# Kernel tuning notes

Measured on AMD Instinct MI355X. Metric: run time of the kernel, lower is better.

The kernel has to match this reference:

```python
import jax, jax.numpy as jnp
import numpy as np

N = 4096   # num ROIs across the batch (sgdet: ~8 images x 512 proposals)
H = 256    # rl_input_size == rl_hidden_size (hard-coded in __init__)
C = 151    # Visual Genome object classes incl. background


def setup_inputs() -> dict:
    key = jax.random.key(0)
    ks = jax.random.split(key, 7)
    prepro_feat = jax.random.normal(ks[0], (N, H), jnp.float32)
    d = jax.random.uniform(ks[1], (N, C), jnp.float32)
    obj_distributions = d / d.sum(-1, keepdims=True)  # softmax-like class probs
    co_occour = jax.random.uniform(ks[2], (C, C), jnp.float32)
    W_sub = jax.random.normal(ks[3], (H, H), jnp.float32) / np.sqrt(H)
    b_sub = jnp.zeros((H,), jnp.float32)
    W_obj = jax.random.normal(ks[4], (H, H), jnp.float32) / np.sqrt(H)
    b_obj = jnp.zeros((H,), jnp.float32)
    w_scores = jax.random.normal(ks[5], (3 * H + 3,), jnp.float32) / np.sqrt(3 * H + 3)
    b_scores = jnp.zeros((), jnp.float32)
    return dict(prepro_feat=prepro_feat, obj_distributions=obj_distributions,
                co_occour=co_occour, W_sub=W_sub, b_sub=b_sub,
                W_obj=W_obj, b_obj=b_obj, w_scores=w_scores, b_scores=b_scores)


def reference(prepro_feat, obj_distributions, co_occour, W_sub, b_sub,
              W_obj, b_obj, w_scores, b_scores):
    n = prepro_feat.shape[0]
    h = W_sub.shape[1]
    # label_scores = co_occour.sum(1)
    label_scores = co_occour.sum(1)                                   # [C]
    # rl_sub/rl_obj Linear + ReLU. In the torch expand, pair (i,j) uses sub[j], obj[i].
    sub = jax.nn.relu(prepro_feat @ W_sub + b_sub)                    # [N,H]
    obj = jax.nn.relu(prepro_feat @ W_obj + b_obj)                    # [N,H]
    # pair_score[i,j] = sum_{a,b} dist[j,a] * dist[i,b] * co[a,b]  (detached)
    pair_score = jax.lax.stop_gradient(
        jnp.einsum('ja,ab,ib->ij', obj_distributions, co_occour, obj_distributions))  # [N,N]
    s = jax.lax.stop_gradient(obj_distributions @ label_scores)       # [N]
    sub_score = s[None, :]   # varies along j
    obj_score = s[:, None]   # varies along i
    # rl_scores Linear over concat(sub*obj, sub, obj, pair, sub_score, obj_score),
    # decomposed exactly into its blocks (avoids the [N,N,3H+3] intermediate).
    w_mul, w_s, w_o = w_scores[:h], w_scores[h:2 * h], w_scores[2 * h:3 * h]
    w_ps, w_ss, w_os = w_scores[3 * h], w_scores[3 * h + 1], w_scores[3 * h + 2]
    pair_out = ((obj * w_mul) @ sub.T                                 # [i,j] = sum_h obj[i,h]*sub[j,h]*w_mul[h]
                + (sub @ w_s)[None, :]
                + (obj @ w_o)[:, None]
                + w_ps * pair_score + w_ss * sub_score + w_os * obj_score
                + b_scores)                                           # [N,N]
    pair_gates = jax.nn.sigmoid(pair_out).reshape(-1, 1)              # [N*N, 1]
    return pair_gates
```

## Files before the change

### kernel.cpp

```cpp
#include <hip/hip_runtime.h>
#include <hip/hip_bf16.h>
#include <math.h>

#define N_DIM 4096
#define H_DIM 256
#define C_DIM 151
#define KP    448
#define KT    160

typedef unsigned short ushort_t;
typedef __attribute__((ext_vector_type(8))) short bf16x8;
typedef __attribute__((ext_vector_type(4))) float f32x4;

#define WSB_PPACK  0
#define WSB_WT     2097152
#define WSB_DPACK  2359296
#define WSB_COT    3670016
#define WSB_PART   3731456
#define WSB_SPART  3993600
#define WSB_APACK  4091904
#define WSB_BPACK  7761920

#define GLL(src, dst) __builtin_amdgcn_global_load_lds( \
    (const __attribute__((address_space(1))) void*)(src), \
    (__attribute__((address_space(3))) void*)(dst), 16, 0, 0)

__global__ __launch_bounds__(256) void k_cvt(
    const float* __restrict__ P, const float* __restrict__ Ws,
    const float* __restrict__ Wo, const float* __restrict__ D,
    const float* __restrict__ co, const float* __restrict__ wsc,
    __hip_bfloat16* __restrict__ Pp, __hip_bfloat16* __restrict__ Wt,
    __hip_bfloat16* __restrict__ Dpack, __hip_bfloat16* __restrict__ coT,
    __hip_bfloat16* __restrict__ Apack) {
    __shared__ float shbuf[64 * C_DIM];
    const int t = threadIdx.x;
    const int bid = blockIdx.x;
    if (bid < 512) {
        int idx = (bid * 256 + t) * 8;
        float4 a = *(const float4*)(P + idx);
        float4 b = *(const float4*)(P + idx + 4);
        __hip_bfloat16 h[8];
        h[0] = __float2bfloat16(a.x); h[1] = __float2bfloat16(a.y);
        h[2] = __float2bfloat16(a.z); h[3] = __float2bfloat16(a.w);
        h[4] = __float2bfloat16(b.x); h[5] = __float2bfloat16(b.y);
        h[6] = __float2bfloat16(b.z); h[7] = __float2bfloat16(b.w);
        *(bf16x8*)&Pp[idx] = *(bf16x8*)h;
    } else if (bid < 544) {
        const int b  = bid - 512;
        const int k0 = (b & 3) * 64;
        const int h0 = ((b >> 2) & 3) * 64;
        const int z  = b >> 4;
        const float* W = z ? Wo : Ws;
        #pragma unroll
        for (int q = 0; q < 4; ++q) {
            int r = (t >> 4) + q * 16;
            int c = (t & 15) * 4;
            float4 f = *(const float4*)&W[(size_t)(k0 + r) * H_DIM + h0 + c];
            shbuf[r * 65 + c] = f.x; shbuf[r * 65 + c + 1] = f.y;
            shbuf[r * 65 + c + 2] = f.z; shbuf[r * 65 + c + 3] = f.w;
        }
        __syncthreads();
        #pragma unroll
        for (int q = 0; q < 2; ++q) {
            int idx = t + q * 256;
            int h   = idx >> 3;
            int kc  = idx & 7;
            __hip_bfloat16 u[8];
            #pragma unroll
            for (int j = 0; j < 8; ++j)
                u[j] = __float2bfloat16(shbuf[(kc * 8 + j) * 65 + h]);
            *(bf16x8*)&Wt[((size_t)z * H_DIM + h0 + h) * H_DIM + k0 + kc * 8] = *(bf16x8*)u;
        }
    } else if (bid < 608) {
        const int b  = bid - 544;
        const int i0 = b * 64;
        for (int idx = t; idx < 64 * C_DIM; idx += 256)
            shbuf[idx] = D[(size_t)i0 * C_DIM + idx];
        __syncthreads();
        const float wps = wsc[768];
        for (int o = t; o < 64 * (KT / 8); o += 256) {
            int r = o / (KT / 8), ch = o % (KT / 8);
            __hip_bfloat16 u[8];
            #pragma unroll
            for (int j = 0; j < 8; ++j) {
                int k = ch * 8 + j;
                u[j] = __float2bfloat16(k < C_DIM ? shbuf[r * C_DIM + k] : 0.f);
            }
            *(bf16x8*)&Dpack[(size_t)(i0 + r) * KT + ch * 8] = *(bf16x8*)u;
        }
        for (int o = t; o < 64 * 24; o += 256) {
            int r = o / 24, ch = o % 24;
            __hip_bfloat16 u[8];
            #pragma unroll
            for (int j = 0; j < 8; ++j) {
                int c = ch * 8 + j;
                u[j] = __float2bfloat16(c < C_DIM ? wps * shbuf[r * C_DIM + c] : 0.f);
            }
            *(bf16x8*)&Apack[(size_t)(i0 + r) * KP + H_DIM + ch * 8] = *(bf16x8*)u;
        }
    } else {
        const int q  = bid - 608;
        const int a0 = (q % 3) * 64;
        const int c0 = (q / 3) * 64;
        for (int o = t; o < 64 * 64; o += 256) {
            int r = o >> 6, c = o & 63;
            float v = 0.f;
            if (a0 + r < C_DIM && c0 + c < C_DIM)
                v = co[(size_t)(a0 + r) * C_DIM + c0 + c];
            shbuf[r * 65 + c] = v;
        }
        __syncthreads();
        const int nch = (a0 == 128) ? 4 : 8;
        for (int o = t; o < 64 * 8; o += 256) {
            int cl = o >> 3, ch = o & 7;
            if (ch < nch) {
                __hip_bfloat16 u[8];
                #pragma unroll
                for (int j = 0; j < 8; ++j)
                    u[j] = __float2bfloat16(shbuf[(ch * 8 + j) * 65 + cl]);
                *(bf16x8*)&coT[(size_t)(c0 + cl) * KT + a0 + ch * 8] = *(bf16x8*)u;
            }
        }
    }
}

__global__ __launch_bounds__(256) void k_mid(
    const ushort_t* __restrict__ Pp, const ushort_t* __restrict__ Wt,
    const ushort_t* __restrict__ Dpack, const ushort_t* __restrict__ coT,
    const float* __restrict__ bsub, const float* __restrict__ bobj,
    const float* __restrict__ wsc,
    __hip_bfloat16* __restrict__ Apack, __hip_bfloat16* __restrict__ Bpack,
    float* __restrict__ part, float* __restrict__ spart) {
    __shared__ ushort_t As[128 * 256];
    __shared__ ushort_t Bs[64 * 256];

    const int t = threadIdx.x;
    const int w = t >> 6, l = t & 63;
    const int wr = w >> 1, wc = w & 1;
    const int lr = l & 15, g = l >> 4;
    const int bid = blockIdx.x;

    if (bid < 256) {
        const int hblk = bid & 3;
        const int i0   = ((bid >> 2) & 31) * 128;
        const int z    = bid >> 7;
        const int j0   = hblk * 64;
        const float* bias = z ? bobj : bsub;
        const ushort_t* Wz = Wt + (size_t)z * H_DIM * H_DIM;

        #pragma unroll
        for (int r_ = 0; r_ < 16; ++r_) {
            int idx = t + r_ * 256, row = idx >> 5, cl = idx & 31;
            int cs = cl ^ (row & 7);
            GLL(Pp + (size_t)(i0 + row) * H_DIM + cs * 8, &As[idx * 8]);
        }
        #pragma unroll
        for (int r_ = 0; r_ < 8; ++r_) {
            int idx = t + r_ * 256, row = idx >> 5, cl = idx & 31;
            int cs = cl ^ (row & 7);
            GLL(Wz + (size_t)(j0 + row) * H_DIM + cs * 8, &Bs[idx * 8]);
        }
        __syncthreads();

        f32x4 acc[4][2];
        #pragma unroll
        for (int m = 0; m < 4; ++m)
            #pragma unroll
            for (int n = 0; n < 2; ++n) acc[m][n] = f32x4{0.f, 0.f, 0.f, 0.f};

        #pragma unroll
        for (int ks2 = 0; ks2 < 8; ++ks2) {
            bf16x8 a[4], b[2];
            int c = ks2 * 4 + g;
            #pragma unroll
            for (int m = 0; m < 4; ++m) {
                int Rl = wr * 64 + m * 16 + lr;
                int cl = c ^ (Rl & 7);
                a[m] = *(const bf16x8*)&As[(Rl * 32 + cl) * 8];
            }
            #pragma unroll
            for (int n = 0; n < 2; ++n) {
                int Rl = wc * 32 + n * 16 + lr;
                int cl = c ^ (Rl & 7);
                b[n] = *(const bf16x8*)&Bs[(Rl * 32 + cl) * 8];
            }
            #pragma unroll
            for (int m = 0; m < 4; ++m)
                #pragma unroll
                for (int n = 0; n < 2; ++n)
                    acc[m][n] = __builtin_amdgcn_mfma_f32_16x16x32_bf16(
                        a[m], b[n], acc[m][n], 0, 0, 0);
        }

        int hn[2]; float bb[2], wse[2], wmu[2];
        #pragma unroll
        for (int n = 0; n < 2; ++n) {
            hn[n]  = j0 + wc * 32 + n * 16 + lr;
            bb[n]  = bias[hn[n]];
            wse[n] = wsc[(z ? 512 : 256) + hn[n]];
            wmu[n] = wsc[hn[n]];
        }
        float* partq = part + (size_t)(z * 8 + hblk * 2 + wc) * N_DIM;
        #pragma unroll
        for (int m = 0; m < 4; ++m) {
            float p[4] = {0.f, 0.f, 0.f, 0.f};
            #pragma unroll
            for (int n = 0; n < 2; ++n)
                #pragma unroll
                for (int r = 0; r < 4; ++r) {
                    float v = acc[m][n][r] + bb[n];
                    v = v > 0.f ? v : 0.f;
                    int i = i0 + wr * 64 + m * 16 + g * 4 + r;
                    if (z) Apack[(size_t)i * KP + hn[n]] = __float2bfloat16(v * wmu[n]);
                    else   Bpack[(size_t)i * KP + hn[n]] = __float2bfloat16(v);
                    p[r] += v * wse[n];
                }
            #pragma unroll
            for (int r = 0; r < 4; ++r) {
                p[r] += __shfl_xor(p[r], 1);
                p[r] += __shfl_xor(p[r], 2);
                p[r] += __shfl_xor(p[r], 4);
                p[r] += __shfl_xor(p[r], 8);
            }
            if (lr == 0)
                #pragma unroll
                for (int r = 0; r < 4; ++r)
                    partq[i0 + wr * 64 + m * 16 + g * 4 + r] = p[r];
        }
    } else {
        const int q  = bid - 256;
        const int j0 = (q % 3) * 64;
        const int i0 = (q / 3) * 64;

        bf16x8 a[2][5], b[2][5];
        #pragma unroll
        for (int m = 0; m < 2; ++m) {
            const ushort_t* ap = Dpack + (size_t)(i0 + wr * 32 + m * 16 + lr) * KT + g * 8;
            #pragma unroll
            for (int ks = 0; ks < 5; ++ks) a[m][ks] = *(const bf16x8*)(ap + ks * 32);
        }
        #pragma unroll
        for (int n = 0; n < 2; ++n) {
            const ushort_t* bp = coT + (size_t)(j0 + wc * 32 + n * 16 + lr) * KT + g * 8;
            #pragma unroll
            for (int ks = 0; ks < 5; ++ks) b[n][ks] = *(const bf16x8*)(bp + ks * 32);
        }

        f32x4 acc[2][2];
        #pragma unroll
        for (int m = 0; m < 2; ++m)
            #pragma unroll
            for (int n = 0; n < 2; ++n) acc[m][n] = f32x4{0.f, 0.f, 0.f, 0.f};
        #pragma unroll
        for (int ks = 0; ks < 5; ++ks)
            #pragma unroll
            for (int m = 0; m < 2; ++m)
                #pragma unroll
                for (int n = 0; n < 2; ++n)
                    acc[m][n] = __builtin_amdgcn_mfma_f32_16x16x32_bf16(
                        a[m][ks], b[n][ks], acc[m][n], 0, 0, 0);

        float* sp = spart + (size_t)((q % 3) * 2 + wc) * N_DIM;
        #pragma unroll
        for (int m = 0; m < 2; ++m) {
            float p[4] = {0.f, 0.f, 0.f, 0.f};
            #pragma unroll
            for (int n = 0; n < 2; ++n) {
                int col = j0 + wc * 32 + n * 16 + lr;
                #pragma unroll
                for (int r = 0; r < 4; ++r) {
                    int i = i0 + wr * 32 + m * 16 + g * 4 + r;
                    float v = acc[m][n][r];
                    Bpack[(size_t)i * KP + H_DIM + col] = __float2bfloat16(v);
                    p[r] += v;
                }
            }
            #pragma unroll
            for (int r = 0; r < 4; ++r) {
                p[r] += __shfl_xor(p[r], 1);
                p[r] += __shfl_xor(p[r], 2);
                p[r] += __shfl_xor(p[r], 4);
                p[r] += __shfl_xor(p[r], 8);
            }
            if (lr == 0)
                #pragma unroll
                for (int r = 0; r < 4; ++r)
                    sp[i0 + wr * 32 + m * 16 + g * 4 + r] = p[r];
        }
    }
}

__global__ __launch_bounds__(512, 2) void k_main(
    const ushort_t* __restrict__ Apack, const ushort_t* __restrict__ Bpack,
    const float* __restrict__ part, const float* __restrict__ spart,
    const float* __restrict__ wsc, const float* __restrict__ bsc,
    float* __restrict__ out) {
    __shared__ ushort_t pool[2][2][256 * 64];
    __shared__ float rbS[256], cbS[256];

    const int t = threadIdx.x;
    const int w = t >> 6, l = t & 63;
    const int wm = w >> 2, wn = w & 3;
    const int lr = l & 15, g = l >> 4;
    const int bid = blockIdx.x;
    const int swz = (bid & 7) * 32 + (bid >> 3);
    const int i0 = (swz >> 4) * 256;
    const int j0 = (swz & 15) * 256;

#define K_STAGE(buf, ks) do {                                                   \
    _Pragma("unroll")                                                           \
    for (int r_ = 0; r_ < 4; ++r_) {                                            \
        int idx_ = t + r_ * 512, row_ = idx_ >> 3, cl_ = idx_ & 7;              \
        int cs_ = cl_ ^ (row_ & 7);                                             \
        GLL(Apack + (size_t)(i0+row_)*KP + (ks)*64 + cs_*8, &pool[buf][0][idx_*8]); \
        GLL(Bpack + (size_t)(j0+row_)*KP + (ks)*64 + cs_*8, &pool[buf][1][idx_*8]); \
    }                                                                           \
} while (0)

#define K_COMPUTE(cur) do {                                                     \
    _Pragma("unroll")                                                           \
    for (int ks2 = 0; ks2 < 2; ++ks2) {                                         \
        bf16x8 a[8], b[4];                                                      \
        int c = ks2 * 4 + g;                                                    \
        _Pragma("unroll")                                                       \
        for (int m = 0; m < 8; ++m) {                                           \
            int Rl = wm * 128 + m * 16 + lr;                                    \
            int cl = c ^ (Rl & 7);                                              \
            a[m] = *(const bf16x8*)&pool[cur][0][(Rl * 8 + cl) * 8];            \
        }                                                                       \
        _Pragma("unroll")                                                       \
        for (int n = 0; n < 4; ++n) {                                           \
            int Rl = wn * 64 + n * 16 + lr;                                     \
            int cl = c ^ (Rl & 7);                                              \
            b[n] = *(const bf16x8*)&pool[cur][1][(Rl * 8 + cl) * 8];            \
        }                                                                       \
        _Pragma("unroll")                                                       \
        for (int m = 0; m < 8; ++m)                                             \
            _Pragma("unroll")                                                   \
            for (int n = 0; n < 4; ++n)                                         \
                acc[m][n] = __builtin_amdgcn_mfma_f32_16x16x32_bf16(            \
                    a[m], b[n], acc[m][n], 0, 0, 0);                            \
    }                                                                           \
} while (0)

    K_STAGE(0, 0);
    if (t < 256) {
        int i = i0 + t; float r = 0.f, si = 0.f;
        #pragma unroll
        for (int q = 8; q < 16; ++q) r += part[(size_t)q * N_DIM + i];
        #pragma unroll
        for (int q = 0; q < 6; ++q) si += spart[(size_t)q * N_DIM + i];
        rbS[t] = r + wsc[770] * si;
    } else {
        int j = j0 + (t - 256); float c = 0.f, sj = 0.f;
        #pragma unroll
        for (int q = 0; q < 8; ++q) c += part[(size_t)q * N_DIM + j];
        #pragma unroll
        for (int q = 0; q < 6; ++q) sj += spart[(size_t)q * N_DIM + j];
        cbS[t - 256] = c + wsc[769] * sj + bsc[0];
    }
    __syncthreads();

    f32x4 acc[8][4];
    #pragma unroll
    for (int m = 0; m < 8; ++m)
        #pragma unroll
        for (int n = 0; n < 4; ++n) acc[m][n] = f32x4{0.f, 0.f, 0.f, 0.f};

    for (int ks = 0; ks < 6; ++ks) {
        const int cur = ks & 1;
        K_STAGE(cur ^ 1, ks + 1);
        asm volatile("s_waitcnt vmcnt(8)" ::: "memory");
        __builtin_amdgcn_s_barrier();
        __builtin_amdgcn_sched_barrier(0);
        K_COMPUTE(cur);
        __builtin_amdgcn_s_barrier();
        __builtin_amdgcn_sched_barrier(0);
    }
    asm volatile("s_waitcnt vmcnt(0)" ::: "memory");
    __builtin_amdgcn_s_barrier();
    __builtin_amdgcn_sched_barrier(0);
    K_COMPUTE(0);
    __builtin_amdgcn_s_barrier();
    __builtin_amdgcn_sched_barrier(0);
#undef K_STAGE
#undef K_COMPUTE

    float cbv[4];
    #pragma unroll
    for (int n = 0; n < 4; ++n) cbv[n] = cbS[wn * 64 + n * 16 + lr];
    float* OutS = (float*)pool;
    #pragma unroll
    for (int m = 0; m < 8; ++m) {
        #pragma unroll
        for (int n = 0; n < 4; ++n) {
            #pragma unroll
            for (int r = 0; r < 4; ++r) {
                float rb = rbS[wm * 128 + m * 16 + g * 4 + r];
                float v  = acc[m][n][r] + rb + cbv[n];
                float e  = __expf(-v);
                OutS[(wm * 16 + g * 4 + r) * 260 + wn * 64 + n * 16 + lr] =
                    __builtin_amdgcn_rcpf(1.0f + e);
            }
        }
        asm volatile("s_waitcnt lgkmcnt(0)" ::: "memory");
        __builtin_amdgcn_s_barrier();
        __builtin_amdgcn_sched_barrier(0);
        {
            int rl = t >> 4, c16 = t & 15;
            int gr = i0 + (rl >> 4) * 128 + m * 16 + (rl & 15);
            float* op = out + (size_t)gr * N_DIM + j0;
            const float* rp = OutS + rl * 260;
            #pragma unroll
            for (int k = 0; k < 4; ++k) {
                float4 v4 = *(const float4*)(rp + (c16 + 16 * k) * 4);
                *(float4*)(op + (c16 + 16 * k) * 4) = v4;
            }
        }
        __builtin_amdgcn_s_barrier();
        __builtin_amdgcn_sched_barrier(0);
    }
}

extern "C" void kernel_launch(void* const* d_in, const int* in_sizes, int n_in,
                              void* d_out, int out_size, void* d_ws, size_t ws_size,
                              hipStream_t stream) {
    const float* prepro = (const float*)d_in[0];
    const float* D      = (const float*)d_in[1];
    const float* co     = (const float*)d_in[2];
    const float* Wsub   = (const float*)d_in[3];
    const float* bsub   = (const float*)d_in[4];
    const float* Wobj   = (const float*)d_in[5];
    const float* bobj   = (const float*)d_in[6];
    const float* wsc    = (const float*)d_in[7];
    const float* bsc    = (const float*)d_in[8];
    float* out = (float*)d_out;

    char* ws = (char*)d_ws;
    __hip_bfloat16* Ppack = (__hip_bfloat16*)(ws + WSB_PPACK);
    __hip_bfloat16* Wt    = (__hip_bfloat16*)(ws + WSB_WT);
    __hip_bfloat16* Dpack = (__hip_bfloat16*)(ws + WSB_DPACK);
    __hip_bfloat16* coT   = (__hip_bfloat16*)(ws + WSB_COT);
    float* part  = (float*)(ws + WSB_PART);
    float* spart = (float*)(ws + WSB_SPART);
    __hip_bfloat16* Apack = (__hip_bfloat16*)(ws + WSB_APACK);
    __hip_bfloat16* Bpack = (__hip_bfloat16*)(ws + WSB_BPACK);

    k_cvt<<<617, 256, 0, stream>>>(prepro, Wsub, Wobj, D, co, wsc,
                                   Ppack, Wt, Dpack, coT, Apack);
    k_mid<<<448, 256, 0, stream>>>(
        (const ushort_t*)Ppack, (const ushort_t*)Wt,
        (const ushort_t*)Dpack, (const ushort_t*)coT,
        bsub, bobj, wsc, Apack, Bpack, part, spart);
    k_main<<<256, 512, 0, stream>>>(
        (const ushort_t*)Apack, (const ushort_t*)Bpack, part, spart, wsc, bsc, out);
}
```

Before: 49.22 us.

## Interleave chunked global-to-LDS prefetch with MFMA phases in GEMM main loop

Splits each K-stage's async global-to-LDS copy into four chunks (two for B, two for A) and issues them between four MFMA sub-phases, instead of issuing the whole next stage at the top of the iteration. B fragments are kept in registers across the two M-halves, and s_setprio is raised around the MFMA bursts. The aim is to spread memory issue across compute and keep the matrix cores fed. The cost is many more workgroup barriers per iteration, which adds synchronisation overhead. The separate __syncthreads after the bias setup is also dropped.

```diff
diff --git a/kernel.cpp b/kernel.cpp
--- a/kernel.cpp
+++ b/kernel.cpp
@@ -307,43 +307,6 @@
     const int i0 = (swz >> 4) * 256;
     const int j0 = (swz & 15) * 256;
 
-#define K_STAGE(buf, ks) do {                                                   \
-    _Pragma("unroll")                                                           \
-    for (int r_ = 0; r_ < 4; ++r_) {                                            \
-        int idx_ = t + r_ * 512, row_ = idx_ >> 3, cl_ = idx_ & 7;              \
-        int cs_ = cl_ ^ (row_ & 7);                                             \
-        GLL(Apack + (size_t)(i0+row_)*KP + (ks)*64 + cs_*8, &pool[buf][0][idx_*8]); \
-        GLL(Bpack + (size_t)(j0+row_)*KP + (ks)*64 + cs_*8, &pool[buf][1][idx_*8]); \
-    }                                                                           \
-} while (0)
-
-#define K_COMPUTE(cur) do {                                                     \
-    _Pragma("unroll")                                                           \
-    for (int ks2 = 0; ks2 < 2; ++ks2) {                                         \
-        bf16x8 a[8], b[4];                                                      \
-        int c = ks2 * 4 + g;                                                    \
-        _Pragma("unroll")                                                       \
-        for (int m = 0; m < 8; ++m) {                                           \
-            int Rl = wm * 128 + m * 16 + lr;                                    \
-            int cl = c ^ (Rl & 7);                                              \
-            a[m] = *(const bf16x8*)&pool[cur][0][(Rl * 8 + cl) * 8];            \
-        }                                                                       \
-        _Pragma("unroll")                                                       \
-        for (int n = 0; n < 4; ++n) {                                           \
-            int Rl = wn * 64 + n * 16 + lr;                                     \
-            int cl = c ^ (Rl & 7);                                              \
-            b[n] = *(const bf16x8*)&pool[cur][1][(Rl * 8 + cl) * 8];            \
-        }                                                                       \
-        _Pragma("unroll")                                                       \
-        for (int m = 0; m < 8; ++m)                                             \
-            _Pragma("unroll")                                                   \
-            for (int n = 0; n < 4; ++n)                                         \
-                acc[m][n] = __builtin_amdgcn_mfma_f32_16x16x32_bf16(            \
-                    a[m], b[n], acc[m][n], 0, 0, 0);                            \
-    }                                                                           \
-} while (0)
-
-    K_STAGE(0, 0);
     if (t < 256) {
         int i = i0 + t; float r = 0.f, si = 0.f;
         #pragma unroll
@@ -359,7 +322,54 @@
         for (int q = 0; q < 6; ++q) sj += spart[(size_t)q * N_DIM + j];
         cbS[t - 256] = c + wsc[769] * sj + bsc[0];
     }
-    __syncthreads();
+
+#define STAGE_CHUNK(buf, ks, half, ab, basePtr, base0) do {                     \
+    _Pragma("unroll")                                                           \
+    for (int r_ = 0; r_ < 2; ++r_) {                                           \
+        int idx_ = t + (r_ + (half) * 2) * 512;                                 \
+        int row_ = idx_ >> 3, cl_ = idx_ & 7;                                   \
+        int cs_ = cl_ ^ (row_ & 7);                                             \
+        GLL(basePtr + (size_t)((base0) + row_) * KP + (ks) * 64 + cs_ * 8,      \
+            &pool[buf][ab][idx_ * 8]);                                          \
+    }                                                                           \
+} while (0)
+
+#define DS_B(ks2) do {                                                          \
+    _Pragma("unroll")                                                           \
+    for (int n_ = 0; n_ < 4; ++n_) {                                            \
+        int Rl = wn * 64 + n_ * 16 + lr;                                        \
+        int cl = ((ks2) * 4 + g) ^ (Rl & 7);                                    \
+        breg[ks2][n_] = *(const bf16x8*)&pool[cur][1][(Rl * 8 + cl) * 8];       \
+    }                                                                           \
+} while (0)
+
+#define DS_A(mh, ks2) do {                                                      \
+    _Pragma("unroll")                                                           \
+    for (int m_ = 0; m_ < 4; ++m_) {                                            \
+        int Rl = wm * 128 + (mh) * 64 + m_ * 16 + lr;                           \
+        int cl = ((ks2) * 4 + g) ^ (Rl & 7);                                    \
+        areg[m_] = *(const bf16x8*)&pool[cur][0][(Rl * 8 + cl) * 8];            \
+    }                                                                           \
+} while (0)
+
+#define MFMA16(mh, ks2) do {                                                    \
+    __builtin_amdgcn_s_setprio(1);                                              \
+    _Pragma("unroll")                                                           \
+    for (int m_ = 0; m_ < 4; ++m_)                                              \
+        _Pragma("unroll")                                                       \
+        for (int n_ = 0; n_ < 4; ++n_)                                          \
+            acc[(mh) * 4 + m_][n_] = __builtin_amdgcn_mfma_f32_16x16x32_bf16(   \
+                areg[m_], breg[ks2][n_], acc[(mh) * 4 + m_][n_], 0, 0, 0);      \
+    __builtin_amdgcn_s_setprio(0);                                              \
+} while (0)
+
+#define BAR() do { __builtin_amdgcn_s_barrier();                                \
+                   __builtin_amdgcn_sched_barrier(0); } while (0)
+
+    STAGE_CHUNK(0, 0, 0, 1, Bpack, j0);
+    STAGE_CHUNK(0, 0, 1, 1, Bpack, j0);
+    STAGE_CHUNK(0, 0, 0, 0, Apack, i0);
+    STAGE_CHUNK(0, 0, 1, 0, Apack, i0);
 
     f32x4 acc[8][4];
     #pragma unroll
@@ -367,24 +377,39 @@
         #pragma unroll
         for (int n = 0; n < 4; ++n) acc[m][n] = f32x4{0.f, 0.f, 0.f, 0.f};
 
-    for (int ks = 0; ks < 6; ++ks) {
-        const int cur = ks & 1;
-        K_STAGE(cur ^ 1, ks + 1);
-        asm volatile("s_waitcnt vmcnt(8)" ::: "memory");
-        __builtin_amdgcn_s_barrier();
-        __builtin_amdgcn_sched_barrier(0);
-        K_COMPUTE(cur);
-        __builtin_amdgcn_s_barrier();
-        __builtin_amdgcn_sched_barrier(0);
+    bf16x8 breg[2][4];
+    bf16x8 areg[4];
+
+    #pragma unroll 1
+    for (int tt = 0; tt < 7; ++tt) {
+        const int cur = tt & 1, nxt = cur ^ 1;
+        const bool pf = (tt < 6);
+        if (pf) {
+            STAGE_CHUNK(nxt, tt + 1, 0, 1, Bpack, j0);
+            asm volatile("s_waitcnt vmcnt(2)" ::: "memory");
+        } else {
+            asm volatile("s_waitcnt vmcnt(0)" ::: "memory");
+        }
+        BAR();
+        DS_B(0); DS_A(0, 0); MFMA16(0, 0);
+        BAR();
+        if (pf) STAGE_CHUNK(nxt, tt + 1, 1, 1, Bpack, j0);
+        BAR();
+        DS_B(1); DS_A(0, 1); MFMA16(0, 1);
+        BAR();
+        if (pf) STAGE_CHUNK(nxt, tt + 1, 0, 0, Apack, i0);
+        BAR();
+        DS_A(1, 0); MFMA16(1, 0);
+        BAR();
+        if (pf) STAGE_CHUNK(nxt, tt + 1, 1, 0, Apack, i0);
+        BAR();
+        DS_A(1, 1); MFMA16(1, 1);
+        BAR();
     }
-    asm volatile("s_waitcnt vmcnt(0)" ::: "memory");
-    __builtin_amdgcn_s_barrier();
-    __builtin_amdgcn_sched_barrier(0);
-    K_COMPUTE(0);
-    __builtin_amdgcn_s_barrier();
-    __builtin_amdgcn_sched_barrier(0);
-#undef K_STAGE
-#undef K_COMPUTE
+#undef STAGE_CHUNK
+#undef DS_B
+#undef DS_A
+#undef MFMA16
 
     float cbv[4];
     #pragma unroll
@@ -404,8 +429,7 @@
             }
         }
         asm volatile("s_waitcnt lgkmcnt(0)" ::: "memory");
-        __builtin_amdgcn_s_barrier();
-        __builtin_amdgcn_sched_barrier(0);
+        BAR();
         {
             int rl = t >> 4, c16 = t & 15;
             int gr = i0 + (rl >> 4) * 128 + m * 16 + (rl & 15);
@@ -417,9 +441,9 @@
                 *(float4*)(op + (c16 + 16 * k) * 4) = v4;
             }
         }
-        __builtin_amdgcn_s_barrier();
-        __builtin_amdgcn_sched_barrier(0);
+        BAR();
     }
+#undef BAR
 }
 
 extern "C" void kernel_launch(void* const* d_in, const int* in_sizes, int n_in,
```

Result: slower. 56.31 us (+14.4%).
